# Optimization experiments

Measured on AMD Instinct MI355X. Metric: run time of the kernel, lower is better.

Reference implementation:

```python
import jax, jax.numpy as jnp
import numpy as np

B, C, L = 32, 512, 4096
H, K = 8, 3            # heads, kernel_size
D = C // H             # head dim
G = 32                 # GroupNorm groups
PAD = (K - 1) // 2
EPS = 1e-5
NEG = -1e30


def setup_inputs() -> dict:
    key = jax.random.key(0)
    ks = jax.random.split(key, 7)
    s = 0.02
    return {
        "x": jax.random.normal(ks[0], (B, C, L), dtype=jnp.float32),
        "gamma": jnp.ones((C,), dtype=jnp.float32),
        "beta": jnp.zeros((C,), dtype=jnp.float32),
        "W_k": jax.random.normal(ks[1], (C, H * D), dtype=jnp.float32) * s,
        "W_v": jax.random.normal(ks[2], (C, H * D), dtype=jnp.float32) * s,
        "W_o": jax.random.normal(ks[3], (H * D, C), dtype=jnp.float32) * s,
        "q": jax.random.normal(ks[4], (H, D), dtype=jnp.float32) * s,     # learned queries (QnA)
        "rpe": jax.random.normal(ks[5], (H, K), dtype=jnp.float32) * s,   # relative-position bias
    }


def _group_norm(x, gamma, beta):
    # x: (B, C, L); normalize over (C//G, L) within each of G groups
    b, c, l = x.shape
    xg = x.reshape(b, G, (c // G) * l)
    mu = jnp.mean(xg, axis=-1, keepdims=True)
    var = jnp.var(xg, axis=-1, keepdims=True)
    xn = ((xg - mu) * jax.lax.rsqrt(var + EPS)).reshape(b, c, l)
    return xn * gamma[None, :, None] + beta[None, :, None]


def reference(x, gamma, beta, W_k, W_v, W_o, q, rpe):
    h = _group_norm(x, gamma, beta)                     # (B, C, L)
    ht = jnp.transpose(h, (0, 2, 1))                    # (B, L, C)
    k = (ht @ W_k).reshape(B, L, H, D)                  # (B, L, H, D)
    v = (ht @ W_v).reshape(B, L, H, D)

    scale = 1.0 / np.sqrt(D).astype(np.float32)
    logits = jnp.einsum('blhd,hd->blh', k, q) * scale   # (B, L, H)

    # sliding windows of size K (zero-padded; -inf logits at boundaries)
    lp = jnp.pad(logits, ((0, 0), (PAD, PAD), (0, 0)), constant_values=NEG)
    lwin = jnp.stack([lp[:, j:j + L] for j in range(K)], axis=2)      # (B, L, K, H)
    lwin = lwin + jnp.transpose(rpe)[None, None]                       # rpe: (H,K)->(K,H)
    attn = jax.nn.softmax(lwin, axis=2)                                # (B, L, K, H)

    vp = jnp.pad(v, ((0, 0), (PAD, PAD), (0, 0), (0, 0)))
    vwin = jnp.stack([vp[:, j:j + L] for j in range(K)], axis=2)       # (B, L, K, H, D)
    o = jnp.einsum('blkh,blkhd->blhd', attn, vwin).reshape(B, L, H * D)

    out = (o @ W_o)                                      # (B, L, C)
    return x + jnp.transpose(out, (0, 2, 1))             # residual, (B, C, L)
```

## Files before the change

### kernel.cpp

```cpp
#include <hip/hip_runtime.h>

#define Bb 32
#define Cc 512
#define Ll 4096
#define Hh 8
#define Dd 64
#define Gg 32
#define BLt (Bb * Ll)
#define NKV 520
#define NKVPAD 640

typedef __attribute__((ext_vector_type(4))) float f32x4;
typedef __attribute__((ext_vector_type(8))) short short8;
typedef __attribute__((ext_vector_type(4))) short s16x4;
typedef __attribute__((ext_vector_type(4))) int int4v;

union U16 { int4v v; short s[8]; };

__device__ __forceinline__ float bf2f(short s) {
    unsigned u = ((unsigned)(unsigned short)s) << 16;
    float f; __builtin_memcpy(&f, &u, 4); return f;
}
__device__ __forceinline__ short f2bf(float f) {
    unsigned u; __builtin_memcpy(&u, &f, 4);
    u = (u + 0x7FFFu + ((u >> 16) & 1u)) >> 16;
    return (short)u;
}

__device__ __forceinline__ int kpack(int k) {
    int blk = k >> 5, r = k & 31;
    return blk * 32 + ((r & 15) >> 2) * 8 + ((r >> 4) << 2) + (r & 3);
}

__device__ __forceinline__ int swz_off(int row, int inner) {
    return row * 128 + (inner ^ ((row & 7) << 4));
}

__device__ __forceinline__ void gload16(const short* g, short* l) {
    __builtin_amdgcn_global_load_lds((const __attribute__((address_space(1))) unsigned int*)g,
                                     (__attribute__((address_space(3))) unsigned int*)l,
                                     16, 0, 0);
}
__device__ __forceinline__ void gload16f(const float* g, float* l) {
    __builtin_amdgcn_global_load_lds((const __attribute__((address_space(1))) unsigned int*)g,
                                     (__attribute__((address_space(3))) unsigned int*)l,
                                     16, 0, 0);
}

#define BAR() __builtin_amdgcn_s_barrier()
#define SFENCE() __builtin_amdgcn_sched_barrier(0)

__global__ void k_prep(const float* __restrict__ Wk, const float* __restrict__ Wv,
                       const float* __restrict__ Wo, const float* __restrict__ q,
                       short* __restrict__ Wct, short* __restrict__ Wot, int packWo)
{
    int bid = blockIdx.x, t = threadIdx.x;
    if (bid < NKVPAD) {
        int n = bid;
        if (n < 512) {
            for (int k = t; k < 512; k += 64)
                Wct[n * 512 + kpack(k)] = f2bf(Wv[k * 512 + n]);
        } else if (n < NKV) {
            int h = n - 512;
            for (int k = t; k < 512; k += 64) {
                float acc = 0.f;
                for (int d = 0; d < 64; ++d)
                    acc += Wk[k * 512 + h * 64 + d] * q[h * 64 + d];
                Wct[n * 512 + kpack(k)] = f2bf(acc * 0.125f);
            }
        } else {
            for (int k = t; k < 512; k += 64) Wct[n * 512 + kpack(k)] = 0;
        }
    } else {
        int c = bid - NKVPAD;
        for (int k = t; k < 512; k += 64)
            Wot[c * 512 + (packWo ? kpack(k) : k)] = f2bf(Wo[k * 512 + c]);
    }
}

__global__ void k_stats(const float* __restrict__ x, float* __restrict__ stats)
{
    int bg = blockIdx.x;
    const float* p = x + (size_t)bg * 65536;
    int t = threadIdx.x;
    float s = 0.f, ss = 0.f;
    for (int i = t * 4; i < 65536; i += 1024) {
        f32x4 v = *(const f32x4*)(p + i);
        s  += v[0] + v[1] + v[2] + v[3];
        ss += v[0]*v[0] + v[1]*v[1] + v[2]*v[2] + v[3]*v[3];
    }
    for (int o = 32; o > 0; o >>= 1) { s += __shfl_down(s, o); ss += __shfl_down(ss, o); }
    __shared__ float red[8];
    int lane = t & 63, w = t >> 6;
    if (lane == 0) { red[w] = s; red[4 + w] = ss; }
    __syncthreads();
    if (t == 0) {
        float S  = red[0] + red[1] + red[2] + red[3];
        float SS = red[4] + red[5] + red[6] + red[7];
        float mean = S * (1.0f / 65536.0f);
        float var  = SS * (1.0f / 65536.0f) - mean * mean;
        stats[bg * 2]     = mean;
        stats[bg * 2 + 1] = rsqrtf(var + 1e-5f);
    }
}

__global__ void k_norm_t(const float* __restrict__ x, const float* __restrict__ gamma,
                         const float* __restrict__ beta, const float* __restrict__ stats,
                         short* __restrict__ hT)
{
    __shared__ float tile[64 * 65];
    int b = blockIdx.z, c0 = blockIdx.y * 64, l0 = blockIdx.x * 64;
    int t = threadIdx.x;
    int lq = t & 15, cq = t >> 4;
    #pragma unroll
    for (int p = 0; p < 4; ++p) {
        int cl = cq + p * 16;
        int c = c0 + cl;
        float mean = stats[(b * 32 + (c >> 4)) * 2];
        float rstd = stats[(b * 32 + (c >> 4)) * 2 + 1];
        float a  = rstd * gamma[c];
        float bb = beta[c] - mean * a;
        f32x4 v = *(const f32x4*)(x + ((size_t)b << 21) + ((size_t)c << 12) + l0 + lq * 4);
        #pragma unroll
        for (int j = 0; j < 4; ++j) tile[cl * 65 + lq * 4 + j] = v[j] * a + bb;
    }
    __syncthreads();
    int ll = t >> 2, cq4 = t & 3;
    int bl = b * Ll + l0 + ll;
    short hbuf[16];
    #pragma unroll
    for (int j = 0; j < 16; ++j) hbuf[j] = f2bf(tile[(cq4 * 16 + j) * 65 + ll]);
    short* dst = hT + (size_t)bl * 512 + ((c0 >> 5) + (cq4 >> 1)) * 32 + ((cq4 & 1) << 2);
    #pragma unroll
    for (int jj = 0; jj < 4; ++jj) {
        s16x4 v4 = { hbuf[jj*4+0], hbuf[jj*4+1], hbuf[jj*4+2], hbuf[jj*4+3] };
        *(s16x4*)(dst + jj * 8) = v4;
    }
}

__launch_bounds__(256, 2)
__global__ void k_gemm1f(const short* __restrict__ A, const short* __restrict__ Bw,
                         short* __restrict__ vbuf, short* __restrict__ lbuf)
{
    __shared__ short sA[2][8192];
    __shared__ short sB[2][8192];
    __shared__ short wqlds[8192];
    const int t = threadIdx.x;
    const int nwg = 1024;
    const int bid = blockIdx.x;
    const int work = (bid & 7) * (nwg >> 3) + (bid >> 3);
    const int ntile = work & 3;
    const int n0 = ntile * 128;
    const int mbase = (work >> 2) * 512;

    const int lane = t & 63, wid = t >> 6;
    const int wm = wid >> 1, wn = wid & 1;
    const int g = lane >> 4, ln = lane & 15;

    {
        int row = t >> 5;
        int cp = (t & 31) * 2;
        int4v v0 = *(const int4v*)(Bw + (size_t)(512 + row) * 512 + cp * 8);
        int4v v1 = *(const int4v*)(Bw + (size_t)(512 + row) * 512 + cp * 8 + 8);
        *(int4v*)((char*)wqlds + row * 1024 + ((cp * 16) ^ ((row & 7) << 4))) = v0;
        *(int4v*)((char*)wqlds + row * 1024 + (((cp + 1) * 16) ^ ((row & 7) << 4))) = v1;
        int4v z = {0, 0, 0, 0};
        int row2 = 8 + (t >> 5);
        *(int4v*)((char*)wqlds + row2 * 1024 + ((cp * 16) ^ ((row2 & 7) << 4))) = z;
        *(int4v*)((char*)wqlds + row2 * 1024 + (((cp + 1) * 16) ^ ((row2 & 7) << 4))) = z;
    }
    asm volatile("s_waitcnt vmcnt(0) lgkmcnt(0)" ::: "memory");
    BAR(); SFENCE();

    const int srow = wid * 8 + (lane >> 3);
    const int sinner = (((lane & 7) ^ ((lane >> 3) & 7)) << 3);
    const short* gAs = A  + (size_t)(mbase + srow) * 512 + sinner;
    const short* gBs = Bw + (size_t)(n0 + srow) * 512 + sinner;

    f32x4 acc[4][4] = {};
    f32x4 accq[4] = {};

    auto stage = [&](int kt, int buf) {
        size_t offA = (size_t)(kt >> 3) * 65536 + (size_t)(kt & 7) * 64;
        size_t offB = (size_t)(kt & 7) * 64;
        #pragma unroll
        for (int gq = 0; gq < 4; ++gq) {
            gload16(gAs + (size_t)gq * 32 * 512 + offA, &sA[buf][gq * 2048 + wid * 512]);
            gload16(gBs + (size_t)gq * 32 * 512 + offB, &sB[buf][gq * 2048 + wid * 512]);
        }
    };
    auto compute = [&](int buf, int kk) {
        #pragma unroll
        for (int ks = 0; ks < 2; ++ks) {
            short8 af[4], bfr[4], bq;
            #pragma unroll
            for (int i = 0; i < 4; ++i) {
                af[i]  = *(const short8*)((const char*)&sA[buf][0] + swz_off(wm * 64 + i * 16 + ln, ks * 64 + g * 16));
                bfr[i] = *(const short8*)((const char*)&sB[buf][0] + swz_off(wn * 64 + i * 16 + ln, ks * 64 + g * 16));
            }
            bq = *(const short8*)((const char*)wqlds + ln * 1024 +
                                  ((kk * 128 + ks * 64 + g * 16) ^ ((ln & 7) << 4)));
            #pragma unroll
            for (int mi = 0; mi < 4; ++mi)
                #pragma unroll
                for (int ni = 0; ni < 4; ++ni)
                    acc[mi][ni] = __builtin_amdgcn_mfma_f32_16x16x32_bf16(af[mi], bfr[ni], acc[mi][ni], 0, 0, 0);
            #pragma unroll
            for (int mi = 0; mi < 4; ++mi)
                accq[mi] = __builtin_amdgcn_mfma_f32_16x16x32_bf16(af[mi], bq, accq[mi], 0, 0, 0);
        }
    };

    stage(0, 0); stage(1, 1);
    #pragma unroll 1
    for (int s = 0; s < 32; ++s) {
        if (s == 31)           asm volatile("s_waitcnt vmcnt(0)"  ::: "memory");
        else if ((s & 7) == 0 && s) asm volatile("s_waitcnt vmcnt(16)" ::: "memory");
        else                   asm volatile("s_waitcnt vmcnt(8)"  ::: "memory");
        BAR(); SFENCE();
        compute(s & 1, s & 7);
        SFENCE();
        if ((s & 7) == 7) {
            BAR();
            int m0 = mbase + (s >> 3) * 128;
            {
                short* scrW = &sB[s & 1][0] + wid * 2048;
                const int blkq = (lane & 7) >> 2, jq = lane & 3;
                #pragma unroll
                for (int p = 0; p < 2; ++p) {
                    #pragma unroll
                    for (int mh = 0; mh < 2; ++mh)
                        #pragma unroll
                        for (int ni = 0; ni < 4; ++ni)
                            #pragma unroll
                            for (int i = 0; i < 4; ++i)
                                scrW[(mh * 16 + g * 4 + i) * 64 + ni * 16 + ln] = f2bf(acc[p * 2 + mh][ni][i]);
                    asm volatile("s_waitcnt lgkmcnt(0)" ::: "memory"); SFENCE();
                    #pragma unroll
                    for (int it = 0; it < 4; ++it) {
                        int mrl = it * 8 + (lane >> 3);
                        const short* bp = scrW + mrl * 64 + blkq * 32;
                        s16x4 lo = *(const s16x4*)(bp + 4 * jq);
                        s16x4 hi = *(const s16x4*)(bp + 16 + 4 * jq);
                        union { int4v v; s16x4 h[2]; } ov;
                        ov.h[0] = lo; ov.h[1] = hi;
                        int m = m0 + wm * 64 + p * 32 + mrl;
                        int nc = n0 + wn * 64 + blkq * 32 + jq * 8;
                        *(int4v*)(vbuf + (size_t)m * 512 + nc) = ov.v;
                    }
                    asm volatile("s_waitcnt lgkmcnt(0)" ::: "memory"); SFENCE();
                }
            }
            if (ntile == 0 && wn == 0 && ln < 8) {
                #pragma unroll
                for (int mi = 0; mi < 4; ++mi)
                    #pragma unroll
                    for (int i = 0; i < 4; ++i) {
                        int m = m0 + wm * 64 + mi * 16 + g * 4 + i;
                        lbuf[(size_t)m * 8 + ln] = f2bf(accq[mi][i]);
                    }
            }
            #pragma unroll
            for (int mi = 0; mi < 4; ++mi) {
                #pragma unroll
                for (int ni = 0; ni < 4; ++ni)
                    acc[mi][ni] = (f32x4){0.f, 0.f, 0.f, 0.f};
                accq[mi] = (f32x4){0.f, 0.f, 0.f, 0.f};
            }
        }
        if (s < 30) { BAR(); stage(s + 2, s & 1); SFENCE(); }
    }
}

__global__ void k_attnw2(const short* __restrict__ lbuf, const float* __restrict__ rpe,
                         float* __restrict__ attnW)
{
    int tid = blockIdx.x * 256 + threadIdx.x;
    int bl = tid >> 3, h = tid & 7;
    int l = bl & (Ll - 1);
    float lg0 = (l > 0)      ? bf2f(lbuf[(size_t)(bl - 1) * 8 + h]) + rpe[h * 3 + 0] : -1e30f;
    float lg1 =                bf2f(lbuf[(size_t)bl * 8 + h])       + rpe[h * 3 + 1];
    float lg2 = (l < Ll - 1) ? bf2f(lbuf[(size_t)(bl + 1) * 8 + h]) + rpe[h * 3 + 2] : -1e30f;
    float m = fmaxf(lg1, fmaxf(lg0, lg2));
    float e0 = (l > 0)      ? __expf(lg0 - m) : 0.f;
    float e1 =                __expf(lg1 - m);
    float e2 = (l < Ll - 1) ? __expf(lg2 - m) : 0.f;
    float inv = 1.0f / (e0 + e1 + e2);
    f32x4 w = { e0 * inv, e1 * inv, e2 * inv, 0.0f };
    *(f32x4*)(attnW + (size_t)bl * 32 + h * 4) = w;
}

__launch_bounds__(256, 2)
__global__ void k_gemm2f(const short* __restrict__ Wot, const short* __restrict__ vbuf,
                         const float* __restrict__ attnW, const float* __restrict__ x,
                         float* __restrict__ out)
{
    __shared__ short sA[2][8192];
    __shared__ short sBc[2][8192];
    __shared__ float wlds[4096];
    const int t = threadIdx.x;
    const int nwg = 1024;
    const int bid = blockIdx.x;
    const int work = (bid & 7) * (nwg >> 3) + (bid >> 3);
    const int n0 = work * 128;

    const int lane = t & 63, wid = t >> 6;
    const int wm = wid >> 1, wn = wid & 1;
    const int g = lane >> 4, ln = lane & 15;

    const int srow = wid * 8 + (lane >> 3);
    const int sinner = (((lane & 7) ^ ((lane >> 3) & 7)) << 3);
    const short* gAs = Wot + (size_t)srow * 512 + sinner;

    const short* gV0[4]; const short* gVm[4]; const short* gVp[4];
    #pragma unroll
    for (int q2 = 0; q2 < 4; ++q2) {
        int r = n0 + srow + 32 * q2;
        int l = r & (Ll - 1);
        int rm = (l == 0) ? r : r - 1;
        int rp = (l == Ll - 1) ? r : r + 1;
        gV0[q2] = vbuf + (size_t)r  * 512 + sinner;
        gVm[q2] = vbuf + (size_t)rm * 512 + sinner;
        gVp[q2] = vbuf + (size_t)rp * 512 + sinner;
    }

    const int r4 = lane >> 4, lcm = (lane & 15) * 4;
    const int ngE = n0 + wn * 64 + lcm;
    const size_t rowbase = ((size_t)(ngE >> 12) << 21) + (size_t)(ngE & (Ll - 1));
    const float* xrow = x + rowbase;
    float* outrow = out + rowbase;

    f32x4 acc[4][4] = {};
    U16 Rm[4], R0[4], Rp[4];

    auto stageA = [&](int s, int buf) {
        size_t off = (size_t)(s >> 3) * 65536 + (size_t)(s & 7) * 64;
        #pragma unroll
        for (int gq = 0; gq < 4; ++gq)
            gload16(gAs + (size_t)gq * 32 * 512 + off, &sA[buf][gq * 2048 + wid * 512]);
    };
    auto loadR = [&](int s1) {
        size_t off = (size_t)(s1 & 7) * 64;
        #pragma unroll
        for (int q2 = 0; q2 < 4; ++q2) {
            Rm[q2].v = *(const int4v*)(gVm[q2] + off);
            R0[q2].v = *(const int4v*)(gV0[q2] + off);
            Rp[q2].v = *(const int4v*)(gVp[q2] + off);
        }
    };
    auto combineStep = [&](int s1, int buf) {
        int h = s1 & 7;
        #pragma unroll
        for (int q2 = 0; q2 < 4; ++q2) {
            int r = srow + 32 * q2;
            f32x4 w = *(const f32x4*)&wlds[r * 32 + ((h ^ (r & 7)) << 2)];
            U16 cm;
            #pragma unroll
            for (int j = 0; j < 8; ++j) {
                float o = w[0] * bf2f(Rm[q2].s[j]) + w[1] * bf2f(R0[q2].s[j])
                        + w[2] * bf2f(Rp[q2].s[j]);
                cm.s[j] = f2bf(o);
            }
            *(int4v*)((char*)&sBc[buf][0] + q2 * 4096 + wid * 1024 + lane * 16) = cm.v;
        }
    };
    auto compute = [&](int buf) {
        #pragma unroll
        for (int ks = 0; ks < 2; ++ks) {
            short8 af[4], bfr[4];
            #pragma unroll
            for (int i = 0; i < 4; ++i) {
                af[i]  = *(const short8*)((const char*)&sA[buf][0] + swz_off(wm * 64 + i * 16 + ln, ks * 64 + g * 16));
                bfr[i] = *(const short8*)((const char*)&sBc[buf][0] + swz_off(wn * 64 + i * 16 + ln, ks * 64 + g * 16));
            }
            #pragma unroll
            for (int mi = 0; mi < 4; ++mi)
                #pragma unroll
                for (int ni = 0; ni < 4; ++ni)
                    acc[mi][ni] = __builtin_amdgcn_mfma_f32_16x16x32_bf16(af[mi], bfr[ni], acc[mi][ni], 0, 0, 0);
        }
    };

    stageA(0, 0); stageA(1, 1);
    {
        const float* wsrc = attnW + (size_t)n0 * 32;
        int rr = lane >> 3, hl = lane & 7;
        #pragma unroll
        for (int j = 0; j < 4; ++j) {
            int row = (wid * 4 + j) * 8 + rr;
            gload16f(wsrc + row * 32 + ((hl ^ (row & 7)) << 2), &wlds[(wid * 4 + j) * 256]);
        }
    }
    loadR(0); SFENCE();
    asm volatile("s_waitcnt vmcnt(0)" ::: "memory");
    BAR(); SFENCE();
    combineStep(0, 0);
    asm volatile("s_waitcnt lgkmcnt(0)" ::: "memory");
    loadR(1); SFENCE();

    #pragma unroll 1
    for (int s = 0; s < 32; ++s) {
        asm volatile("s_waitcnt vmcnt(0)" ::: "memory");
        BAR(); SFENCE();
        if (s < 31) combineStep(s + 1, (s + 1) & 1);
        compute(s & 1);
        asm volatile("s_waitcnt lgkmcnt(0)" ::: "memory"); SFENCE();
        if ((s & 7) == 7) {
            BAR();
            float* scr = (float*)((char*)&sA[s & 1][0] + wid * 4096);
            int m0c = (s >> 3) * 128;
            #pragma unroll
            for (int p = 0; p < 4; ++p) {
                #pragma unroll
                for (int ni = 0; ni < 4; ++ni)
                    #pragma unroll
                    for (int i = 0; i < 4; ++i) {
                        int r = g * 4 + i;
                        int col = (ni * 16 + ln) ^ ((((r & 3) ^ (r >> 2)) & 3) << 4);
                        scr[r * 64 + col] = acc[p][ni][i];
                    }
                asm volatile("s_waitcnt lgkmcnt(0)" ::: "memory"); SFENCE();
                #pragma unroll
                for (int j = 0; j < 4; ++j) {
                    int rr = r4 + 4 * j;
                    int cst = lcm ^ ((((rr & 3) ^ (rr >> 2)) & 3) << 4);
                    f32x4 sv = *(const f32x4*)&scr[rr * 64 + cst];
                    int c = m0c + wm * 64 + p * 16 + rr;
                    f32x4 xv = *(const f32x4*)(xrow + ((size_t)c << 12));
                    *(f32x4*)(outrow + ((size_t)c << 12)) = xv + sv;
                }
                asm volatile("s_waitcnt lgkmcnt(0)" ::: "memory"); SFENCE();
            }
            #pragma unroll
            for (int mi = 0; mi < 4; ++mi)
                #pragma unroll
                for (int ni = 0; ni < 4; ++ni)
                    acc[mi][ni] = (f32x4){0.f, 0.f, 0.f, 0.f};
        }
        if (s < 30) {
            BAR();
            stageA(s + 2, s & 1);
            loadR(s + 2);
            SFENCE();
        }
    }
}

__launch_bounds__(256, 2)
__global__ void k_gemm1_fb(const short* __restrict__ A, const short* __restrict__ Bw,
                           short* __restrict__ kv)
{
    __shared__ short sA[2][8192];
    __shared__ short sB[2][8192];
    const int t = threadIdx.x;
    const int m0 = blockIdx.y * 128;
    const int n0 = blockIdx.x * 128;
    const int lane = t & 63, wid = t >> 6;
    const int wm = wid >> 1, wn = wid & 1;
    const int g = lane >> 4, ln = lane & 15;

    const int srow = wid * 8 + (lane >> 3);
    const int sinner = (((lane & 7) ^ ((lane >> 3) & 7)) << 3);
    const short* gAs = A  + (size_t)(m0 + srow) * 512 + sinner;
    const short* gBs = Bw + (size_t)(n0 + srow) * 512 + sinner;

    f32x4 acc[4][4] = {};

    auto stage = [&](int kt, int buf) {
        #pragma unroll
        for (int gq = 0; gq < 4; ++gq) {
            gload16(gAs + (size_t)gq * 32 * 512 + kt * 64, &sA[buf][gq * 2048 + wid * 512]);
            gload16(gBs + (size_t)gq * 32 * 512 + kt * 64, &sB[buf][gq * 2048 + wid * 512]);
        }
    };
    auto compute = [&](int buf) {
        #pragma unroll
        for (int ks = 0; ks < 2; ++ks) {
            short8 af[4], bfr[4];
            #pragma unroll
            for (int i = 0; i < 4; ++i) {
                af[i]  = *(const short8*)((const char*)&sA[buf][0] + swz_off(wm * 64 + i * 16 + ln, ks * 64 + g * 16));
                bfr[i] = *(const short8*)((const char*)&sB[buf][0] + swz_off(wn * 64 + i * 16 + ln, ks * 64 + g * 16));
            }
            #pragma unroll
            for (int mi = 0; mi < 4; ++mi)
                #pragma unroll
                for (int ni = 0; ni < 4; ++ni)
                    acc[mi][ni] = __builtin_amdgcn_mfma_f32_16x16x32_bf16(af[mi], bfr[ni], acc[mi][ni], 0, 0, 0);
        }
    };

    stage(0, 0);
    __syncthreads();
    #pragma unroll 1
    for (int kt = 0; kt < 8; ++kt) {
        if (kt < 7) stage(kt + 1, (kt + 1) & 1);
        compute(kt & 1);
        __syncthreads();
    }

    #pragma unroll
    for (int mi = 0; mi < 4; ++mi)
        #pragma unroll
        for (int ni = 0; ni < 4; ++ni) {
            int n = n0 + wn * 64 + ni * 16 + ln;
            if (n < NKV) {
                #pragma unroll
                for (int i = 0; i < 4; ++i) {
                    int m = m0 + wm * 64 + mi * 16 + g * 4 + i;
                    kv[(size_t)m * NKV + n] = f2bf(acc[mi][ni][i]);
                }
            }
        }
}

__global__ void k_attnw(const short* __restrict__ kv, const float* __restrict__ rpe,
                        float* __restrict__ attnW)
{
    int tid = blockIdx.x * 256 + threadIdx.x;
    int bl = tid >> 3, h = tid & 7;
    int l = bl & (Ll - 1);
    float lg[3];
    #pragma unroll
    for (int j = 0; j < 3; ++j) {
        bool valid = (j == 1) || (j == 0 && l > 0) || (j == 2 && l < Ll - 1);
        lg[j] = valid ? (bf2f(kv[(size_t)(bl + j - 1) * NKV + 512 + h]) + rpe[h * 3 + j])
                      : -1e30f;
    }
    float m = fmaxf(lg[0], fmaxf(lg[1], lg[2]));
    float e0 = __expf(lg[0] - m), e1 = __expf(lg[1] - m), e2 = __expf(lg[2] - m);
    float inv = 1.0f / (e0 + e1 + e2);
    f32x4 w = { e0 * inv, e1 * inv, e2 * inv, 0.0f };
    *(f32x4*)(attnW + (size_t)bl * 32 + h * 4) = w;
}

__launch_bounds__(256, 2)
__global__ void k_gemm2_fused(const short* __restrict__ Wot, const short* __restrict__ kv,
                              const float* __restrict__ attnW, const float* __restrict__ x,
                              float* __restrict__ out)
{
    __shared__ short sA[2][8192];
    __shared__ short sB[2][8192];
    const int t = threadIdx.x;
    const int m0 = blockIdx.x * 128;
    const int n0 = blockIdx.y * 128;
    const int lane = t & 63, wid = t >> 6;
    const int wm = wid >> 1, wn = wid & 1;
    const int g = lane >> 4, ln = lane & 15;
    const int sr = t >> 1, ksh = t & 1;

    const short* gA = Wot + (size_t)(m0 + sr) * 512 + ksh * 32;
    const int nrow = n0 + sr;
    const int lpos = nrow & (Ll - 1);
    const int nm1 = (lpos == 0) ? nrow : nrow - 1;
    const int np1 = (lpos == Ll - 1) ? nrow : nrow + 1;
    const short* gV0 = kv + (size_t)nrow * NKV + ksh * 32;
    const short* gVm = kv + (size_t)nm1  * NKV + ksh * 32;
    const short* gVp = kv + (size_t)np1  * NKV + ksh * 32;
    const float* gW = attnW + (size_t)nrow * 32;

    f32x4 acc[4][4] = {};
    U16 ra[4], rbm[4], rb0[4], rbp[4];
    f32x4 wv;

    auto load_tile = [&](int kt) {
        #pragma unroll
        for (int qq = 0; qq < 4; ++qq) {
            ra[qq].v  = *(const int4v*)(gA  + kt * 64 + qq * 8);
            rbm[qq].v = *(const int4v*)(gVm + kt * 64 + qq * 8);
            rb0[qq].v = *(const int4v*)(gV0 + kt * 64 + qq * 8);
            rbp[qq].v = *(const int4v*)(gVp + kt * 64 + qq * 8);
        }
        wv = *(const f32x4*)(gW + kt * 4);
    };
    auto write_tile = [&](int buf) {
        short ob[32];
        #pragma unroll
        for (int qq = 0; qq < 4; ++qq)
            #pragma unroll
            for (int j = 0; j < 8; ++j) {
                float o = wv[0] * bf2f(rbm[qq].s[j]) + wv[1] * bf2f(rb0[qq].s[j])
                        + wv[2] * bf2f(rbp[qq].s[j]);
                ob[qq * 8 + j] = f2bf(o);
            }
        #pragma unroll
        for (int f = 0; f < 4; ++f) {
            U16 wa, wb;
            #pragma unroll
            for (int j = 0; j < 4; ++j) {
                wa.s[j]     = ra[f >> 1].s[(f & 1) * 4 + j];
                wa.s[4 + j] = ra[2 + (f >> 1)].s[(f & 1) * 4 + j];
                wb.s[j]     = ob[4 * f + j];
                wb.s[4 + j] = ob[16 + 4 * f + j];
            }
            int off = swz_off(sr, ksh * 64 + f * 16);
            *(int4v*)((char*)&sA[buf][0] + off) = wa.v;
            *(int4v*)((char*)&sB[buf][0] + off) = wb.v;
        }
    };
    auto compute = [&](int buf) {
        #pragma unroll
        for (int ks = 0; ks < 2; ++ks) {
            short8 af[4], bfr[4];
            #pragma unroll
            for (int i = 0; i < 4; ++i) {
                af[i]  = *(const short8*)((const char*)&sA[buf][0] + swz_off(wm * 64 + i * 16 + ln, ks * 64 + g * 16));
                bfr[i] = *(const short8*)((const char*)&sB[buf][0] + swz_off(wn * 64 + i * 16 + ln, ks * 64 + g * 16));
            }
            #pragma unroll
            for (int mi = 0; mi < 4; ++mi)
                #pragma unroll
                for (int ni = 0; ni < 4; ++ni)
                    acc[mi][ni] = __builtin_amdgcn_mfma_f32_16x16x32_bf16(af[mi], bfr[ni], acc[mi][ni], 0, 0, 0);
        }
    };

    load_tile(0); write_tile(0); __syncthreads();
    #pragma unroll 1
    for (int kt = 0; kt < 8; ++kt) {
        if (kt < 7) load_tile(kt + 1);
        compute(kt & 1);
        if (kt < 7) write_tile((kt + 1) & 1);
        __syncthreads();
    }

    #pragma unroll
    for (int mi = 0; mi < 4; ++mi)
        #pragma unroll
        for (int ni = 0; ni < 4; ++ni)
            #pragma unroll
            for (int i = 0; i < 4; ++i) {
                int c = m0 + wm * 64 + mi * 16 + g * 4 + i;
                int ng = n0 + wn * 64 + ni * 16 + ln;
                int b = ng >> 12, l = ng & (Ll - 1);
                size_t off = ((size_t)b << 21) | ((size_t)c << 12) | (size_t)l;
                out[off] = x[off] + acc[mi][ni][i];
            }
}

extern "C" void kernel_launch(void* const* d_in, const int* in_sizes, int n_in,
                              void* d_out, int out_size, void* d_ws, size_t ws_size,
                              hipStream_t stream)
{
    const float* x     = (const float*)d_in[0];
    const float* gamma = (const float*)d_in[1];
    const float* beta  = (const float*)d_in[2];
    const float* Wk    = (const float*)d_in[3];
    const float* Wv    = (const float*)d_in[4];
    const float* Wo    = (const float*)d_in[5];
    const float* q     = (const float*)d_in[6];
    const float* rpe   = (const float*)d_in[7];
    float* out = (float*)d_out;
    char* ws = (char*)d_ws;

    const size_t MB128 = 134217728ull;
    const size_t MAIN_WS = MB128 * 2 + 655360 + 524288 + 2097152 + 8192;

    if (ws_size >= MAIN_WS) {
        float* attnW = (float*)(ws);
        short* vbuf  = (short*)(ws + MB128);
        short* Wct   = (short*)(ws + 2 * MB128);
        short* Wot   = (short*)(ws + 2 * MB128 + 655360);
        short* lbuf  = (short*)(ws + 2 * MB128 + 655360 + 524288);
        float* stats = (float*)(ws + 2 * MB128 + 655360 + 524288 + 2097152);
        short* hT    = (short*)d_out;

        k_prep<<<1152, 64, 0, stream>>>(Wk, Wv, Wo, q, Wct, Wot, 1);
        k_stats<<<1024, 256, 0, stream>>>(x, stats);
        k_norm_t<<<dim3(64, 8, 32), 256, 0, stream>>>(x, gamma, beta, stats, hT);
        k_gemm1f<<<1024, 256, 0, stream>>>(hT, Wct, vbuf, lbuf);
        k_attnw2<<<4096, 256, 0, stream>>>(lbuf, rpe, attnW);
        k_gemm2f<<<1024, 256, 0, stream>>>(Wot, vbuf, attnW, x, out);
    } else {
        short* Wct   = (short*)(ws + 0);
        short* Wot   = (short*)(ws + 655360);
        float* stats = (float*)(ws + 1179648);
        float* attnW = (float*)(ws + 1187840);
        short* kv    = (short*)(ws + 17965056);
        short* hT    = (short*)d_out;

        k_prep<<<1152, 64, 0, stream>>>(Wk, Wv, Wo, q, Wct, Wot, 0);
        k_stats<<<1024, 256, 0, stream>>>(x, stats);
        k_norm_t<<<dim3(64, 8, 32), 256, 0, stream>>>(x, gamma, beta, stats, hT);
        k_gemm1_fb<<<dim3(5, 1024), 256, 0, stream>>>(hT, Wct, kv);
        k_attnw<<<4096, 256, 0, stream>>>(kv, rpe, attnW);
        k_gemm2_fused<<<dim3(4, 1024), 256, 0, stream>>>(Wot, kv, attnW, x, out);
    }
}
```

Baseline: 522.7 us.

## Double-buffer V register loads and use partial vmcnt waits in output GEMM

The output-projection kernel now keeps two register sets of V window rows (A/B) and unrolls the main loop by two. Loads for step s+2 are issued before the combine for step s+1, so each wait can use a partial vmcnt count instead of draining all outstanding loads. V addressing also switches from 64-bit pointers to 32-bit byte offsets to save registers. The cost is more registers per thread and hand-tuned vmcnt counts that must exactly match the number of outstanding loads, or the kernel reads stale data.

```diff
diff --git a/kernel.cpp b/kernel.cpp
--- a/kernel.cpp
+++ b/kernel.cpp
@@ -312,17 +312,18 @@
     const int sinner = (((lane & 7) ^ ((lane >> 3) & 7)) << 3);
     const short* gAs = Wot + (size_t)srow * 512 + sinner;
 
-    const short* gV0[4]; const short* gVm[4]; const short* gVp[4];
+    unsigned ovm[4], ov0[4], ovp[4];
     #pragma unroll
     for (int q2 = 0; q2 < 4; ++q2) {
         int r = n0 + srow + 32 * q2;
         int l = r & (Ll - 1);
         int rm = (l == 0) ? r : r - 1;
         int rp = (l == Ll - 1) ? r : r + 1;
-        gV0[q2] = vbuf + (size_t)r  * 512 + sinner;
-        gVm[q2] = vbuf + (size_t)rm * 512 + sinner;
-        gVp[q2] = vbuf + (size_t)rp * 512 + sinner;
-    }
+        ov0[q2] = (unsigned)r  * 1024u + (unsigned)sinner * 2u;
+        ovm[q2] = (unsigned)rm * 1024u + (unsigned)sinner * 2u;
+        ovp[q2] = (unsigned)rp * 1024u + (unsigned)sinner * 2u;
+    }
+    const char* vb = (const char*)vbuf;
 
     const int r4 = lane >> 4, lcm = (lane & 15) * 4;
     const int ngE = n0 + wn * 64 + lcm;
@@ -331,7 +332,8 @@
     float* outrow = out + rowbase;
 
     f32x4 acc[4][4] = {};
-    U16 Rm[4], R0[4], Rp[4];
+    U16 RAm[4], RA0[4], RAp[4];
+    U16 RBm[4], RB0[4], RBp[4];
 
     auto stageA = [&](int s, int buf) {
         size_t off = (size_t)(s >> 3) * 65536 + (size_t)(s & 7) * 64;
@@ -339,16 +341,16 @@
         for (int gq = 0; gq < 4; ++gq)
             gload16(gAs + (size_t)gq * 32 * 512 + off, &sA[buf][gq * 2048 + wid * 512]);
     };
-    auto loadR = [&](int s1) {
-        size_t off = (size_t)(s1 & 7) * 64;
+    auto loadRto = [&](U16 (&Rm_)[4], U16 (&R0_)[4], U16 (&Rp_)[4], int s1) {
+        unsigned off = (unsigned)(s1 & 7) * 128u;
         #pragma unroll
         for (int q2 = 0; q2 < 4; ++q2) {
-            Rm[q2].v = *(const int4v*)(gVm[q2] + off);
-            R0[q2].v = *(const int4v*)(gV0[q2] + off);
-            Rp[q2].v = *(const int4v*)(gVp[q2] + off);
-        }
-    };
-    auto combineStep = [&](int s1, int buf) {
+            Rm_[q2].v = *(const int4v*)(vb + ovm[q2] + off);
+            R0_[q2].v = *(const int4v*)(vb + ov0[q2] + off);
+            Rp_[q2].v = *(const int4v*)(vb + ovp[q2] + off);
+        }
+    };
+    auto combineFrom = [&](U16 (&Rm_)[4], U16 (&R0_)[4], U16 (&Rp_)[4], int s1, int buf) {
         int h = s1 & 7;
         #pragma unroll
         for (int q2 = 0; q2 < 4; ++q2) {
@@ -357,8 +359,8 @@
             U16 cm;
             #pragma unroll
             for (int j = 0; j < 8; ++j) {
-                float o = w[0] * bf2f(Rm[q2].s[j]) + w[1] * bf2f(R0[q2].s[j])
-                        + w[2] * bf2f(Rp[q2].s[j]);
+                float o = w[0] * bf2f(Rm_[q2].s[j]) + w[1] * bf2f(R0_[q2].s[j])
+                        + w[2] * bf2f(Rp_[q2].s[j]);
                 cm.s[j] = f2bf(o);
             }
             *(int4v*)((char*)&sBc[buf][0] + q2 * 4096 + wid * 1024 + lane * 16) = cm.v;
@@ -379,6 +381,38 @@
                 for (int ni = 0; ni < 4; ++ni)
                     acc[mi][ni] = __builtin_amdgcn_mfma_f32_16x16x32_bf16(af[mi], bfr[ni], acc[mi][ni], 0, 0, 0);
         }
+    };
+    auto epilogue = [&](int s) {
+        BAR();
+        float* scr = (float*)((char*)&sA[s & 1][0] + wid * 4096);
+        int m0c = (s >> 3) * 128;
+        #pragma unroll
+        for (int p = 0; p < 4; ++p) {
+            #pragma unroll
+            for (int ni = 0; ni < 4; ++ni)
+                #pragma unroll
+                for (int i = 0; i < 4; ++i) {
+                    int r = g * 4 + i;
+                    int col = (ni * 16 + ln) ^ ((((r & 3) ^ (r >> 2)) & 3) << 4);
+                    scr[r * 64 + col] = acc[p][ni][i];
+                }
+            asm volatile("s_waitcnt lgkmcnt(0)" ::: "memory"); SFENCE();
+            #pragma unroll
+            for (int j = 0; j < 4; ++j) {
+                int rr = r4 + 4 * j;
+                int cst = lcm ^ ((((rr & 3) ^ (rr >> 2)) & 3) << 4);
+                f32x4 sv = *(const f32x4*)&scr[rr * 64 + cst];
+                int c = m0c + wm * 64 + p * 16 + rr;
+                f32x4 xv = *(const f32x4*)(xrow + ((size_t)c << 12));
+                *(f32x4*)(outrow + ((size_t)c << 12)) = xv + sv;
+            }
+            asm volatile("s_waitcnt lgkmcnt(0)" ::: "memory"); SFENCE();
+        }
+        #pragma unroll
+        for (int mi = 0; mi < 4; ++mi)
+            #pragma unroll
+            for (int ni = 0; ni < 4; ++ni)
+                acc[mi][ni] = (f32x4){0.f, 0.f, 0.f, 0.f};
     };
 
     stageA(0, 0); stageA(1, 1);
@@ -391,57 +425,38 @@
             gload16f(wsrc + row * 32 + ((hl ^ (row & 7)) << 2), &wlds[(wid * 4 + j) * 256]);
         }
     }
-    loadR(0); SFENCE();
+    loadRto(RAm, RA0, RAp, 0); SFENCE();
     asm volatile("s_waitcnt vmcnt(0)" ::: "memory");
     BAR(); SFENCE();
-    combineStep(0, 0);
-    asm volatile("s_waitcnt lgkmcnt(0)" ::: "memory");
-    loadR(1); SFENCE();
+    combineFrom(RAm, RA0, RAp, 0, 0);
+    asm volatile("s_waitcnt lgkmcnt(0)" ::: "memory"); SFENCE();
+    loadRto(RBm, RB0, RBp, 1); SFENCE();
 
     #pragma unroll 1
-    for (int s = 0; s < 32; ++s) {
-        asm volatile("s_waitcnt vmcnt(0)" ::: "memory");
-        BAR(); SFENCE();
-        if (s < 31) combineStep(s + 1, (s + 1) & 1);
-        compute(s & 1);
-        asm volatile("s_waitcnt lgkmcnt(0)" ::: "memory"); SFENCE();
-        if ((s & 7) == 7) {
-            BAR();
-            float* scr = (float*)((char*)&sA[s & 1][0] + wid * 4096);
-            int m0c = (s >> 3) * 128;
-            #pragma unroll
-            for (int p = 0; p < 4; ++p) {
-                #pragma unroll
-                for (int ni = 0; ni < 4; ++ni)
-                    #pragma unroll
-                    for (int i = 0; i < 4; ++i) {
-                        int r = g * 4 + i;
-                        int col = (ni * 16 + ln) ^ ((((r & 3) ^ (r >> 2)) & 3) << 4);
-                        scr[r * 64 + col] = acc[p][ni][i];
-                    }
-                asm volatile("s_waitcnt lgkmcnt(0)" ::: "memory"); SFENCE();
-                #pragma unroll
-                for (int j = 0; j < 4; ++j) {
-                    int rr = r4 + 4 * j;
-                    int cst = lcm ^ ((((rr & 3) ^ (rr >> 2)) & 3) << 4);
-                    f32x4 sv = *(const f32x4*)&scr[rr * 64 + cst];
-                    int c = m0c + wm * 64 + p * 16 + rr;
-                    f32x4 xv = *(const f32x4*)(xrow + ((size_t)c << 12));
-                    *(f32x4*)(outrow + ((size_t)c << 12)) = xv + sv;
-                }
-                asm volatile("s_waitcnt lgkmcnt(0)" ::: "memory"); SFENCE();
-            }
-            #pragma unroll
-            for (int mi = 0; mi < 4; ++mi)
-                #pragma unroll
-                for (int ni = 0; ni < 4; ++ni)
-                    acc[mi][ni] = (f32x4){0.f, 0.f, 0.f, 0.f};
-        }
-        if (s < 30) {
-            BAR();
-            stageA(s + 2, s & 1);
-            loadR(s + 2);
-            SFENCE();
+    for (int ss = 0; ss < 16; ++ss) {
+        {
+            const int se = 2 * ss;
+            if (se < 30) { loadRto(RAm, RA0, RAp, se + 2); SFENCE(); }
+            if (se == 30)            asm volatile("s_waitcnt vmcnt(16)" ::: "memory");
+            else if ((se & 7) == 0 && se) asm volatile("s_waitcnt vmcnt(44)" ::: "memory");
+            else                     asm volatile("s_waitcnt vmcnt(28)" ::: "memory");
+            BAR(); SFENCE();
+            combineFrom(RBm, RB0, RBp, se + 1, 1);
+            compute(0);
+            asm volatile("s_waitcnt lgkmcnt(0)" ::: "memory"); SFENCE();
+            if (se < 30) { BAR(); stageA(se + 2, 0); SFENCE(); }
+        }
+        {
+            const int so = 2 * ss + 1;
+            if (so < 30) { loadRto(RBm, RB0, RBp, so + 2); SFENCE(); }
+            if (so == 31) asm volatile("s_waitcnt vmcnt(0)"  ::: "memory");
+            else          asm volatile("s_waitcnt vmcnt(28)" ::: "memory");
+            BAR(); SFENCE();
+            if (so < 31) combineFrom(RAm, RA0, RAp, so + 1, 0);
+            compute(1);
+            asm volatile("s_waitcnt lgkmcnt(0)" ::: "memory"); SFENCE();
+            if ((so & 7) == 7) epilogue(so);
+            if (so < 30) { BAR(); stageA(so + 2, 1); SFENCE(); }
         }
     }
 }
```

Result: slower. 719.3 us (+37.6%).

## Issue V-row prefetch earlier and use partial vmcnt waits in output GEMM

Applied to the files above, without the earlier changes.

In the fused combine + W_o GEMM kernel, the next step's neighbour V-row register loads are now issued right after the current combine step, not after compute. The full vmcnt(0) wait at each iteration becomes a partial count, so outstanding loads stay in flight across the barrier. Per-row 64-bit pointers become 32-bit byte offsets to save registers, and the epilogue moves into a lambda. The hand-tuned vmcnt counts depend on the exact number and order of issued memory ops, so a miscount could cause a data race.

```diff
diff --git a/kernel.cpp b/kernel.cpp
--- a/kernel.cpp
+++ b/kernel.cpp
@@ -312,17 +312,18 @@
     const int sinner = (((lane & 7) ^ ((lane >> 3) & 7)) << 3);
     const short* gAs = Wot + (size_t)srow * 512 + sinner;
 
-    const short* gV0[4]; const short* gVm[4]; const short* gVp[4];
+    unsigned ovm[4], ov0[4], ovp[4];
     #pragma unroll
     for (int q2 = 0; q2 < 4; ++q2) {
         int r = n0 + srow + 32 * q2;
         int l = r & (Ll - 1);
         int rm = (l == 0) ? r : r - 1;
         int rp = (l == Ll - 1) ? r : r + 1;
-        gV0[q2] = vbuf + (size_t)r  * 512 + sinner;
-        gVm[q2] = vbuf + (size_t)rm * 512 + sinner;
-        gVp[q2] = vbuf + (size_t)rp * 512 + sinner;
-    }
+        ov0[q2] = (unsigned)r  * 1024u + (unsigned)sinner * 2u;
+        ovm[q2] = (unsigned)rm * 1024u + (unsigned)sinner * 2u;
+        ovp[q2] = (unsigned)rp * 1024u + (unsigned)sinner * 2u;
+    }
+    const char* vb = (const char*)vbuf;
 
     const int r4 = lane >> 4, lcm = (lane & 15) * 4;
     const int ngE = n0 + wn * 64 + lcm;
@@ -340,12 +341,12 @@
             gload16(gAs + (size_t)gq * 32 * 512 + off, &sA[buf][gq * 2048 + wid * 512]);
     };
     auto loadR = [&](int s1) {
-        size_t off = (size_t)(s1 & 7) * 64;
+        unsigned off = (unsigned)(s1 & 7) * 128u;
         #pragma unroll
         for (int q2 = 0; q2 < 4; ++q2) {
-            Rm[q2].v = *(const int4v*)(gVm[q2] + off);
-            R0[q2].v = *(const int4v*)(gV0[q2] + off);
-            Rp[q2].v = *(const int4v*)(gVp[q2] + off);
+            Rm[q2].v = *(const int4v*)(vb + ovm[q2] + off);
+            R0[q2].v = *(const int4v*)(vb + ov0[q2] + off);
+            Rp[q2].v = *(const int4v*)(vb + ovp[q2] + off);
         }
     };
     auto combineStep = [&](int s1, int buf) {
@@ -380,6 +381,38 @@
                     acc[mi][ni] = __builtin_amdgcn_mfma_f32_16x16x32_bf16(af[mi], bfr[ni], acc[mi][ni], 0, 0, 0);
         }
     };
+    auto epilogue = [&](int s) {
+        BAR();
+        float* scr = (float*)((char*)&sA[s & 1][0] + wid * 4096);
+        int m0c = (s >> 3) * 128;
+        #pragma unroll
+        for (int p = 0; p < 4; ++p) {
+            #pragma unroll
+            for (int ni = 0; ni < 4; ++ni)
+                #pragma unroll
+                for (int i = 0; i < 4; ++i) {
+                    int r = g * 4 + i;
+                    int col = (ni * 16 + ln) ^ ((((r & 3) ^ (r >> 2)) & 3) << 4);
+                    scr[r * 64 + col] = acc[p][ni][i];
+                }
+            asm volatile("s_waitcnt lgkmcnt(0)" ::: "memory"); SFENCE();
+            #pragma unroll
+            for (int j = 0; j < 4; ++j) {
+                int rr = r4 + 4 * j;
+                int cst = lcm ^ ((((rr & 3) ^ (rr >> 2)) & 3) << 4);
+                f32x4 sv = *(const f32x4*)&scr[rr * 64 + cst];
+                int c = m0c + wm * 64 + p * 16 + rr;
+                f32x4 xv = *(const f32x4*)(xrow + ((size_t)c << 12));
+                *(f32x4*)(outrow + ((size_t)c << 12)) = xv + sv;
+            }
+            asm volatile("s_waitcnt lgkmcnt(0)" ::: "memory"); SFENCE();
+        }
+        #pragma unroll
+        for (int mi = 0; mi < 4; ++mi)
+            #pragma unroll
+            for (int ni = 0; ni < 4; ++ni)
+                acc[mi][ni] = (f32x4){0.f, 0.f, 0.f, 0.f};
+    };
 
     stageA(0, 0); stageA(1, 1);
     {
@@ -395,54 +428,24 @@
     asm volatile("s_waitcnt vmcnt(0)" ::: "memory");
     BAR(); SFENCE();
     combineStep(0, 0);
-    asm volatile("s_waitcnt lgkmcnt(0)" ::: "memory");
+    asm volatile("s_waitcnt lgkmcnt(0)" ::: "memory"); SFENCE();
     loadR(1); SFENCE();
 
     #pragma unroll 1
     for (int s = 0; s < 32; ++s) {
-        asm volatile("s_waitcnt vmcnt(0)" ::: "memory");
+        if (s == 0 || s == 31)       asm volatile("s_waitcnt vmcnt(0)"  ::: "memory");
+        else if ((s & 7) == 0)       asm volatile("s_waitcnt vmcnt(36)" ::: "memory");
+        else                         asm volatile("s_waitcnt vmcnt(4)"  ::: "memory");
         BAR(); SFENCE();
-        if (s < 31) combineStep(s + 1, (s + 1) & 1);
+        if (s < 31) {
+            combineStep(s + 1, (s + 1) & 1);
+            SFENCE();
+            if (s < 30) { loadR(s + 2); SFENCE(); }
+        }
         compute(s & 1);
         asm volatile("s_waitcnt lgkmcnt(0)" ::: "memory"); SFENCE();
-        if ((s & 7) == 7) {
-            BAR();
-            float* scr = (float*)((char*)&sA[s & 1][0] + wid * 4096);
-            int m0c = (s >> 3) * 128;
-            #pragma unroll
-            for (int p = 0; p < 4; ++p) {
-                #pragma unroll
-                for (int ni = 0; ni < 4; ++ni)
-                    #pragma unroll
-                    for (int i = 0; i < 4; ++i) {
-                        int r = g * 4 + i;
-                        int col = (ni * 16 + ln) ^ ((((r & 3) ^ (r >> 2)) & 3) << 4);
-                        scr[r * 64 + col] = acc[p][ni][i];
-                    }
-                asm volatile("s_waitcnt lgkmcnt(0)" ::: "memory"); SFENCE();
-                #pragma unroll
-                for (int j = 0; j < 4; ++j) {
-                    int rr = r4 + 4 * j;
-                    int cst = lcm ^ ((((rr & 3) ^ (rr >> 2)) & 3) << 4);
-                    f32x4 sv = *(const f32x4*)&scr[rr * 64 + cst];
-                    int c = m0c + wm * 64 + p * 16 + rr;
-                    f32x4 xv = *(const f32x4*)(xrow + ((size_t)c << 12));
-                    *(f32x4*)(outrow + ((size_t)c << 12)) = xv + sv;
-                }
-                asm volatile("s_waitcnt lgkmcnt(0)" ::: "memory"); SFENCE();
-            }
-            #pragma unroll
-            for (int mi = 0; mi < 4; ++mi)
-                #pragma unroll
-                for (int ni = 0; ni < 4; ++ni)
-                    acc[mi][ni] = (f32x4){0.f, 0.f, 0.f, 0.f};
-        }
-        if (s < 30) {
-            BAR();
-            stageA(s + 2, s & 1);
-            loadR(s + 2);
-            SFENCE();
-        }
+        if ((s & 7) == 7) epilogue(s);
+        if (s < 30) { BAR(); stageA(s + 2, s & 1); SFENCE(); }
     }
 }
 
```

Measured after the change: 509.8 us. -2.5%, faster.
